# Performance work log

Measured on AMD Instinct MI355X. Metric: run time of the kernel, lower is better.

## Reference

```python
import jax, jax.numpy as jnp
import numpy as np

RADIUS, HMIN, HMAX, NSAMPLE = 0.05, -0.02, 0.04, 32
EPS = 1e-5


def setup_inputs() -> dict:
    key = jax.random.key(0)
    ks = jax.random.split(key, 6)
    B, N, C, OUT = 4, 2048, 256, 256
    seed_xyz_graspable = jax.random.uniform(ks[0], (B, N, 3), jnp.float32) * 0.2
    seed_features_graspable = jax.random.normal(ks[1], (B, C, N), jnp.float32)
    vp_rot = jax.random.normal(ks[2], (B, N, 3, 3), jnp.float32)
    W1 = jax.random.normal(ks[3], (OUT, 3 + C), jnp.float32) * 0.02
    W2 = jax.random.normal(ks[4], (OUT, OUT), jnp.float32) * 0.02
    return {
        "seed_xyz_graspable": seed_xyz_graspable,
        "seed_features_graspable": seed_features_graspable,
        "vp_rot": vp_rot,
        "W1": W1, "gamma1": jnp.ones((OUT,), jnp.float32), "beta1": jnp.zeros((OUT,), jnp.float32),
        "W2": W2, "gamma2": jnp.ones((OUT,), jnp.float32), "beta2": jnp.zeros((OUT,), jnp.float32),
    }


def _cylinder_query(xyz, rot):
    # xyz: (B,N,3), rot: (B,N,3,3); new_xyz == xyz.
    B, N, _ = xyz.shape
    d = xyz[:, None, :, :] - xyz[:, :, None, :]                  # (B,P,N,3) offsets to each candidate
    r = jnp.einsum('bpij,bpnj->bpni', rot, d)                    # rotate into cylinder frame (rot @ d)
    mask = (r[..., 1] ** 2 + r[..., 2] ** 2 < RADIUS ** 2) & (r[..., 0] > HMIN) & (r[..., 0] < HMAX)
    order = jnp.arange(N, dtype=jnp.int32)
    keys = jnp.where(mask, order, order + N)                     # in-cylinder points sort first, stable order
    _, idx = jax.lax.top_k(-keys, NSAMPLE)                       # first NSAMPLE indices satisfying the query
    valid = jnp.take_along_axis(mask, idx, axis=-1)
    first = idx[..., :1]
    any_valid = valid[..., :1]
    idx = jnp.where(valid, idx, jnp.where(any_valid, first, 0))  # pad with first hit like the CUDA kernel
    return idx                                                   # (B,P,NSAMPLE) int32


def _group(xyz, features, rot, idx):
    gxyz = jax.vmap(lambda a, i: a[i])(xyz, idx)                 # (B,P,S,3)
    gxyz = (gxyz - xyz[:, :, None, :]) / RADIUS                  # center on query + normalize_xyz
    gxyz = jnp.einsum('bpsj,bpjk->bpsk', gxyz, rot)              # rotate_xyz: grouped_xyz @ rot
    gfeat = jax.vmap(lambda f, i: f[:, i])(features, idx)        # (B,C,P,S)
    return jnp.concatenate([gxyz.transpose(0, 3, 1, 2), gfeat], axis=1)  # (B,3+C,P,S)


def _conv_bn_relu(x, W, gamma, beta):
    y = jnp.einsum('oc,bcps->bops', W, x)                        # 1x1 conv, no bias (bn=True)
    mu = y.mean(axis=(0, 2, 3), keepdims=True)
    var = y.var(axis=(0, 2, 3), keepdims=True)
    y = (y - mu) * jax.lax.rsqrt(var + EPS)
    y = y * gamma[None, :, None, None] + beta[None, :, None, None]
    return jax.nn.relu(y)


def reference(seed_xyz_graspable, seed_features_graspable, vp_rot, W1, gamma1, beta1, W2, gamma2, beta2):
    idx = _cylinder_query(seed_xyz_graspable, vp_rot)
    g = _group(seed_xyz_graspable, seed_features_graspable, vp_rot, idx)
    h = _conv_bn_relu(g, W1, gamma1, beta1)
    h = _conv_bn_relu(h, W2, gamma2, beta2)
    return h.max(axis=3)                                         # maxpool over nsample -> (B,OUT,P)
```

## Files before the change

### kernel.cpp

```cpp
#include <hip/hip_runtime.h>

typedef unsigned short u16;
typedef unsigned int u32;
typedef __attribute__((ext_vector_type(8))) short bf16x8;
typedef __attribute__((ext_vector_type(4))) float f32x4;

#define NPTS 2048
#define CFEAT 256
#define NS 32
#define MTOT 262144
#define GRID1 2048
#define GRID2 4096
#define INV_N (1.0f/262144.0f)

__device__ __forceinline__ float bf2f(u16 u) {
    union { u32 i; float f; } v; v.i = ((u32)u) << 16; return v.f;
}
__device__ __forceinline__ u16 f2bf(float f) {
    union { float f; u32 i; } v; v.f = f;
    u32 i = v.i;
    return (u16)((i + 0x7fffu + ((i >> 16) & 1u)) >> 16);
}

__device__ __forceinline__ void stage1k(u16* lds, const u16* g, int lane) {
    __builtin_amdgcn_global_load_lds((const __attribute__((address_space(1))) void*)(g + lane * 8),
                                     (__attribute__((address_space(3))) void*)lds, 16, 0, 0);
}

__global__ __launch_bounds__(256) void prep_k(const float* __restrict__ W1, const float* __restrict__ W2,
                                              u16* __restrict__ Wp1T, u16* __restrict__ Wp2T) {
    int o = blockIdx.x, t = threadIdx.x;
    int ks = t >> 5, kc = t & 31;
    Wp1T[(ks * 256 + o) * 32 + kc] = f2bf(W1[o * 259 + 3 + t]);
    Wp2T[(ks * 256 + o) * 32 + kc] = f2bf(W2[o * 256 + t]);
    if (t < 32) Wp1T[(8 * 256 + o) * 32 + t] = (t < 3) ? f2bf(W1[o * 259 + t]) : (u16)0;
}

__global__ __launch_bounds__(256) void query_k(const float* __restrict__ xyz, const float* __restrict__ rot,
                                               int* __restrict__ idx) {
    int pid = blockIdx.x * 4 + (threadIdx.x >> 6);
    int lane = threadIdx.x & 63;
    int b = pid >> 11, p = pid & 2047;
    const float* xb = xyz + (size_t)b * NPTS * 3;
    float px = xb[p * 3 + 0], py = xb[p * 3 + 1], pz = xb[p * 3 + 2];
    const float* rp = rot + (size_t)pid * 9;
    float r00 = rp[0], r01 = rp[1], r02 = rp[2];
    float r10 = rp[3], r11 = rp[4], r12 = rp[5];
    float r20 = rp[6], r21 = rp[7], r22 = rp[8];
    int cnt = 0, first = 0;
    for (int n0 = 0; n0 < NPTS && cnt < NS; n0 += 64) {
        int n = n0 + lane;
        float dx = __fsub_rn(xb[n * 3 + 0], px);
        float dy = __fsub_rn(xb[n * 3 + 1], py);
        float dz = __fsub_rn(xb[n * 3 + 2], pz);
        float a0 = __fadd_rn(__fadd_rn(__fmul_rn(r00, dx), __fmul_rn(r01, dy)), __fmul_rn(r02, dz));
        float a1 = __fadd_rn(__fadd_rn(__fmul_rn(r10, dx), __fmul_rn(r11, dy)), __fmul_rn(r12, dz));
        float a2 = __fadd_rn(__fadd_rn(__fmul_rn(r20, dx), __fmul_rn(r21, dy)), __fmul_rn(r22, dz));
        float t2 = __fadd_rn(__fmul_rn(a1, a1), __fmul_rn(a2, a2));
        bool valid = (t2 < 0.0025f) && (a0 > -0.02f) && (a0 < 0.04f);
        unsigned long long bal = __ballot(valid);
        if (cnt == 0 && bal) first = n0 + __builtin_ctzll(bal);
        int rank = __builtin_popcountll(bal & ((1ull << lane) - 1ull));
        int slot = cnt + rank;
        if (valid && slot < NS) idx[(size_t)pid * NS + slot] = n;
        cnt += __builtin_popcountll(bal);
    }
    int filled = cnt < NS ? cnt : NS;
    if (lane >= filled && lane < NS) idx[(size_t)pid * NS + lane] = (cnt > 0) ? first : 0;
}

__global__ __launch_bounds__(256) void featT_k(const float* __restrict__ feat, u16* __restrict__ featT) {
    __shared__ float sm[32 * 33];
    int b = blockIdx.z;
    int n0 = blockIdx.x * 32, c0 = blockIdx.y * 32;
    int t = threadIdx.x, x = t & 31, y = t >> 5;
    #pragma unroll
    for (int rr = 0; rr < 4; rr++) {
        int c = c0 + y + rr * 8;
        sm[(y + rr * 8) * 33 + x] = feat[((size_t)(b * CFEAT + c)) * NPTS + n0 + x];
    }
    __syncthreads();
    #pragma unroll
    for (int rr = 0; rr < 4; rr++) {
        int n = n0 + y + rr * 8;
        featT[((size_t)(b * NPTS + n)) * CFEAT + c0 + x] = f2bf(sm[x * 33 + (y + rr * 8)]);
    }
}

__global__ __launch_bounds__(256) void gxyz_k(const float* __restrict__ xyz, const float* __restrict__ rot,
                                              const int* __restrict__ idx, u16* __restrict__ gxyz) {
    int m = blockIdx.x * 256 + threadIdx.x;
    int pid = m >> 5;
    int b = pid >> 11, p = pid & 2047;
    int i = idx[m];
    const float* xb = xyz + (size_t)b * NPTS * 3;
    float dx = (xb[i * 3 + 0] - xb[p * 3 + 0]) * 20.0f;
    float dy = (xb[i * 3 + 1] - xb[p * 3 + 1]) * 20.0f;
    float dz = (xb[i * 3 + 2] - xb[p * 3 + 2]) * 20.0f;
    const float* rp = rot + (size_t)pid * 9;
    float g0 = dx * rp[0] + dy * rp[3] + dz * rp[6];
    float g1 = dx * rp[1] + dy * rp[4] + dz * rp[7];
    float g2 = dx * rp[2] + dy * rp[5] + dz * rp[8];
    uint2 v;
    v.x = (u32)f2bf(g0) | ((u32)f2bf(g1) << 16);
    v.y = (u32)f2bf(g2);
    *(uint2*)(gxyz + (size_t)m * 4) = v;
}

#define ASTR 40
__global__ __launch_bounds__(256, 2) void gemm1_k(
    const u16* __restrict__ featT, const u16* __restrict__ gxyz, const int* __restrict__ idx,
    const u16* __restrict__ Wp1T, float* __restrict__ psum, float* __restrict__ psq,
    uint2* __restrict__ y1f)
{
    __shared__ __attribute__((aligned(16))) u16 As[2][128 * ASTR];
    __shared__ __attribute__((aligned(16))) u16 Bs[2][8192];
    __shared__ int rowb[128];

    const int tid = threadIdx.x;
    const int lane = tid & 63, wave = tid >> 6;
    const int quad = lane >> 4, tl = lane & 15;
    const int wm = (wave & 1) * 64, wn = (wave >> 1) * 128;
    const int bx = blockIdx.x;
    const int m0 = bx * 128;
    const int srow = tid >> 1, shalf = tid & 1;

    if (tid < 128) {
        int m = m0 + tid;
        rowb[tid] = (m >> 16) * (NPTS * CFEAT) + idx[m] * CFEAT;
    }
    __syncthreads();

    {
        const u16* p = featT + rowb[srow] + shalf * 16;
        *(uint4*)(&As[0][srow * ASTR + shalf * 16]) = *(const uint4*)p;
        *(uint4*)(&As[0][srow * ASTR + shalf * 16 + 8]) = *(const uint4*)(p + 8);
    }
    #pragma unroll
    for (int c = 0; c < 4; c++)
        stage1k(&Bs[0][wave * 2048 + c * 512], Wp1T + wave * 2048 + c * 512, lane);

    f32x4 acc[4][8];
    #pragma unroll
    for (int i = 0; i < 4; i++)
        #pragma unroll
        for (int j = 0; j < 8; j++) acc[i][j] = (f32x4){0.f, 0.f, 0.f, 0.f};

    for (int ks = 0; ks < 9; ks++) {
        __syncthreads();
        const u16* Ab = As[ks & 1];
        const u16* Bb = Bs[ks & 1];
        bf16x8 af[4], bv[8];
        #pragma unroll
        for (int i = 0; i < 4; i++)
            af[i] = *(const bf16x8*)(Ab + (wm + i * 16 + tl) * ASTR + quad * 8);
        #pragma unroll
        for (int j = 0; j < 8; j++)
            bv[j] = *(const bf16x8*)(Bb + (wn + j * 16 + tl) * 32 + quad * 8);
        if (ks < 8) {
            u16* An = As[(ks + 1) & 1];
            u16* Bn = Bs[(ks + 1) & 1];
            const u16* gsrc = Wp1T + (ks + 1) * 8192;
            #pragma unroll
            for (int c = 0; c < 4; c++)
                stage1k(Bn + wave * 2048 + c * 512, gsrc + wave * 2048 + c * 512, lane);
            uint4 v0, v1;
            if (ks + 1 < 8) {
                const u16* p = featT + rowb[srow] + (ks + 1) * 32 + shalf * 16;
                v0 = *(const uint4*)p; v1 = *(const uint4*)(p + 8);
            } else {
                v0 = make_uint4(0, 0, 0, 0); v1 = v0;
                if (shalf == 0) {
                    uint2 g2 = *(const uint2*)(gxyz + (size_t)(m0 + srow) * 4);
                    v0.x = g2.x; v0.y = g2.y;
                }
            }
            *(uint4*)(An + srow * ASTR + shalf * 16) = v0;
            *(uint4*)(An + srow * ASTR + shalf * 16 + 8) = v1;
        }
        #pragma unroll
        for (int j = 0; j < 8; j++)
            #pragma unroll
            for (int i = 0; i < 4; i++)
                acc[i][j] = __builtin_amdgcn_mfma_f32_16x16x32_bf16(af[i], bv[j], acc[i][j], 0, 0, 0);
    }

    const int mb = bx * 2 + (wave & 1);
    #pragma unroll
    for (int j = 0; j < 8; j++) {
        const int cb = (wave >> 1) * 2 + (j >> 2);
        float s = 0.f, q2 = 0.f;
        #pragma unroll
        for (int i = 0; i < 4; i++) {
            float v0 = acc[i][j][0], v1 = acc[i][j][1], v2 = acc[i][j][2], v3 = acc[i][j][3];
            u32 lo = (u32)f2bf(v0) | ((u32)f2bf(v1) << 16);
            u32 hi = (u32)f2bf(v2) | ((u32)f2bf(v3) << 16);
            y1f[(((size_t)mb * 4 + cb) * 16 + i * 4 + (j & 3)) * 64 + lane] = make_uint2(lo, hi);
            v0 = bf2f((u16)(lo & 0xffff)); v1 = bf2f((u16)(lo >> 16));
            v2 = bf2f((u16)(hi & 0xffff)); v3 = bf2f((u16)(hi >> 16));
            s += v0 + v1 + v2 + v3;
            q2 += v0 * v0 + v1 * v1 + v2 * v2 + v3 * v3;
        }
        s += __shfl_xor(s, 16); s += __shfl_xor(s, 32);
        q2 += __shfl_xor(q2, 16); q2 += __shfl_xor(q2, 32);
        if (quad == 0) {
            int col = wn + j * 16 + tl;
            psum[(size_t)mb * 256 + col] = s;
            psq[(size_t)mb * 256 + col] = q2;
        }
    }
}

__global__ __launch_bounds__(256, 3) void gemm2_k(
    const uint2* __restrict__ y1f, const u16* __restrict__ Wp2T, const float* __restrict__ ab1,
    float* __restrict__ psum, float* __restrict__ psq,
    float* __restrict__ ymax, float* __restrict__ ymin)
{
    __shared__ __attribute__((aligned(16))) u16 Bs[8192];
    __shared__ __attribute__((aligned(16))) u16 y1s[64 * 264];
    const int tid = threadIdx.x;
    const int lane = tid & 63, wave = tid >> 6;
    const int quad = lane >> 4, tl = lane & 15;
    const int bx = blockIdx.x;

    #pragma unroll
    for (int j = 0; j < 4; j++) {
        int col = wave * 64 + j * 16 + tl;
        float a = ab1[col], bb = ab1[256 + col];
        #pragma unroll
        for (int i = 0; i < 4; i++) {
            uint2 v = y1f[((size_t)(bx * 4 + wave) * 16 + i * 4 + j) * 64 + lane];
            float f0 = bf2f((u16)(v.x & 0xffff)), f1 = bf2f((u16)(v.x >> 16));
            float f2 = bf2f((u16)(v.y & 0xffff)), f3 = bf2f((u16)(v.y >> 16));
            int rbi = (i * 16 + quad * 4) * 264 + col;
            y1s[rbi] = f2bf(fmaxf(fmaf(f0, a, bb), 0.f));
            y1s[rbi + 264] = f2bf(fmaxf(fmaf(f1, a, bb), 0.f));
            y1s[rbi + 528] = f2bf(fmaxf(fmaf(f2, a, bb), 0.f));
            y1s[rbi + 792] = f2bf(fmaxf(fmaf(f3, a, bb), 0.f));
        }
    }

    f32x4 acc2[4][4];
    #pragma unroll
    for (int i = 0; i < 4; i++)
        #pragma unroll
        for (int j = 0; j < 4; j++) acc2[i][j] = (f32x4){0.f, 0.f, 0.f, 0.f};

    for (int ks = 0; ks < 8; ks++) {
        const u16* gsrc = Wp2T + ks * 8192;
        #pragma unroll
        for (int c = 0; c < 4; c++)
            stage1k(Bs + wave * 2048 + c * 512, gsrc + wave * 2048 + c * 512, lane);
        __syncthreads();
        bf16x8 afv[4], bv[4];
        #pragma unroll
        for (int i = 0; i < 4; i++) afv[i] = *(const bf16x8*)(y1s + (i * 16 + tl) * 264 + ks * 32 + quad * 8);
        #pragma unroll
        for (int j = 0; j < 4; j++) bv[j] = *(const bf16x8*)(Bs + (wave * 64 + j * 16 + tl) * 32 + quad * 8);
        #pragma unroll
        for (int i = 0; i < 4; i++)
            #pragma unroll
            for (int j = 0; j < 4; j++)
                acc2[i][j] = __builtin_amdgcn_mfma_f32_16x16x32_bf16(afv[i], bv[j], acc2[i][j], 0, 0, 0);
        if (ks < 7) __syncthreads();
    }

    #pragma unroll
    for (int j = 0; j < 4; j++) {
        int col = wave * 64 + j * 16 + tl;
        float s = 0.f, q2 = 0.f;
        float mx0 = -3.0e38f, mn0 = 3.0e38f, mx1 = -3.0e38f, mn1 = 3.0e38f;
        #pragma unroll
        for (int i = 0; i < 4; i++)
            #pragma unroll
            for (int r = 0; r < 4; r++) {
                float v = acc2[i][j][r];
                s += v; q2 += v * v;
                if (i < 2) { mx0 = fmaxf(mx0, v); mn0 = fminf(mn0, v); }
                else       { mx1 = fmaxf(mx1, v); mn1 = fminf(mn1, v); }
            }
        s += __shfl_xor(s, 16); s += __shfl_xor(s, 32);
        q2 += __shfl_xor(q2, 16); q2 += __shfl_xor(q2, 32);
        mx0 = fmaxf(mx0, __shfl_xor(mx0, 16)); mx0 = fmaxf(mx0, __shfl_xor(mx0, 32));
        mn0 = fminf(mn0, __shfl_xor(mn0, 16)); mn0 = fminf(mn0, __shfl_xor(mn0, 32));
        mx1 = fmaxf(mx1, __shfl_xor(mx1, 16)); mx1 = fmaxf(mx1, __shfl_xor(mx1, 32));
        mn1 = fminf(mn1, __shfl_xor(mn1, 16)); mn1 = fminf(mn1, __shfl_xor(mn1, 32));
        if (quad == 0) {
            psum[(size_t)bx * 256 + col] = s;
            psq[(size_t)bx * 256 + col] = q2;
            size_t p0 = (size_t)(bx * 2) * 256 + col;
            size_t p1 = (size_t)(bx * 2 + 1) * 256 + col;
            ymax[p0] = mx0; ymin[p0] = mn0;
            ymax[p1] = mx1; ymin[p1] = mn1;
        }
    }
}

__global__ __launch_bounds__(256) void reduce_k(const float* __restrict__ psum, const float* __restrict__ psq,
                                                const float* __restrict__ gamma, const float* __restrict__ beta,
                                                float* __restrict__ ab) {
    __shared__ float red[8];
    int c = blockIdx.x, t = threadIdx.x;
    float s = 0.f, q = 0.f;
    for (int k = t; k < 4096; k += 256) { s += psum[(size_t)k * 256 + c]; q += psq[(size_t)k * 256 + c]; }
    #pragma unroll
    for (int o = 32; o >= 1; o >>= 1) { s += __shfl_xor(s, o); q += __shfl_xor(q, o); }
    int lane = t & 63, w = t >> 6;
    if (lane == 0) { red[w] = s; red[4 + w] = q; }
    __syncthreads();
    if (t == 0) {
        float S = red[0] + red[1] + red[2] + red[3];
        float Q = red[4] + red[5] + red[6] + red[7];
        float mu = S * INV_N;
        float var = Q * INV_N - mu * mu;
        float a = gamma[c] * rsqrtf(var + 1e-5f);
        ab[c] = a;
        ab[256 + c] = beta[c] - mu * a;
    }
}

__global__ __launch_bounds__(256) void final_k(const float* __restrict__ ymax, const float* __restrict__ ymin,
                                               const float* __restrict__ ab, float* __restrict__ out) {
    __shared__ float sm[32 * 33];
    int b = blockIdx.z;
    int n0 = blockIdx.x * 32, o0 = blockIdx.y * 32;
    int t = threadIdx.x, x = t & 31, y = t >> 5;
    #pragma unroll
    for (int rr = 0; rr < 4; rr++) {
        int n = n0 + y + rr * 8;
        int o = o0 + x;
        float a = ab[o], bb = ab[256 + o];
        size_t p = (size_t)(b * NPTS + n) * 256 + o;
        float v = (a >= 0.f) ? ymax[p] : ymin[p];
        sm[(y + rr * 8) * 33 + x] = fmaxf(fmaf(v, a, bb), 0.f);
    }
    __syncthreads();
    #pragma unroll
    for (int rr = 0; rr < 4; rr++)
        out[((size_t)(b * 256 + o0 + y + rr * 8)) * NPTS + n0 + x] = sm[x * 33 + (y + rr * 8)];
}

extern "C" void kernel_launch(void* const* d_in, const int* in_sizes, int n_in,
                              void* d_out, int out_size, void* d_ws, size_t ws_size,
                              hipStream_t stream) {
    const float* xyz    = (const float*)d_in[0];
    const float* feat   = (const float*)d_in[1];
    const float* rot    = (const float*)d_in[2];
    const float* W1     = (const float*)d_in[3];
    const float* gamma1 = (const float*)d_in[4];
    const float* beta1  = (const float*)d_in[5];
    const float* W2     = (const float*)d_in[6];
    const float* gamma2 = (const float*)d_in[7];
    const float* beta2  = (const float*)d_in[8];
    float* out = (float*)d_out;

    char* ws = (char*)d_ws;
    u16*   featT = (u16*)(ws + 0);
    int*   idx   = (int*)(ws + 4194304);
    u16*   gxyz  = (u16*)(ws + 5242880);
    u16*   Wp1T  = (u16*)(ws + 7340032);
    u16*   Wp2T  = (u16*)(ws + 7487488);
    float* ab1   = (float*)(ws + 7618560);
    float* ab2   = (float*)(ws + 7620608);
    float* psum  = (float*)(ws + 7622656);
    float* psq   = (float*)(ws + 11816960);
    float* ymax  = (float*)(ws + 16011264);
    float* ymin  = (float*)(ws + 24399872);
    uint2* y1f   = (uint2*)(ws + 32788480);

    prep_k<<<256, 256, 0, stream>>>(W1, W2, Wp1T, Wp2T);
    query_k<<<2048, 256, 0, stream>>>(xyz, rot, idx);
    featT_k<<<dim3(64, 8, 4), 256, 0, stream>>>(feat, featT);
    gxyz_k<<<1024, 256, 0, stream>>>(xyz, rot, idx, gxyz);

    gemm1_k<<<GRID1, 256, 0, stream>>>(featT, gxyz, idx, Wp1T, psum, psq, y1f);
    reduce_k<<<256, 256, 0, stream>>>(psum, psq, gamma1, beta1, ab1);
    gemm2_k<<<GRID2, 256, 0, stream>>>(y1f, Wp2T, ab1, psum, psq, ymax, ymin);
    reduce_k<<<256, 256, 0, stream>>>(psum, psq, gamma2, beta2, ab2);
    final_k<<<dim3(64, 8, 4), 256, 0, stream>>>(ymax, ymin, ab2, out);
}
```

Baseline: 257.4 us.

## Fuse gxyz into gemm1 and retile gemm2 with pipelined K-sliced y1 layout

The separate gxyz kernel is removed and its rotated neighbour offsets are computed inside gemm1 and kept in shared memory. gemm1 now writes y1 through shared memory into a K-sliced row-major layout. gemm2 is retiled to 128x256 blocks with double-buffered A and B staging, applying BN1 and ReLU while staging. This cuts a kernel launch and the gxyz round trip, and aims for better MFMA reuse in gemm2, at the cost of a larger gemm1 epilogue and more LDS and register pressure.

```diff
diff --git a/kernel.cpp b/kernel.cpp
--- a/kernel.cpp
+++ b/kernel.cpp
@@ -10,8 +10,9 @@
 #define NS 32
 #define MTOT 262144
 #define GRID1 2048
-#define GRID2 4096
 #define INV_N (1.0f/262144.0f)
+#define ASTR 40
+#define YSTR 260
 
 __device__ __forceinline__ float bf2f(u16 u) {
     union { u32 i; float f; } v; v.i = ((u32)u) << 16; return v.f;
@@ -87,35 +88,17 @@
     }
 }
 
-__global__ __launch_bounds__(256) void gxyz_k(const float* __restrict__ xyz, const float* __restrict__ rot,
-                                              const int* __restrict__ idx, u16* __restrict__ gxyz) {
-    int m = blockIdx.x * 256 + threadIdx.x;
-    int pid = m >> 5;
-    int b = pid >> 11, p = pid & 2047;
-    int i = idx[m];
-    const float* xb = xyz + (size_t)b * NPTS * 3;
-    float dx = (xb[i * 3 + 0] - xb[p * 3 + 0]) * 20.0f;
-    float dy = (xb[i * 3 + 1] - xb[p * 3 + 1]) * 20.0f;
-    float dz = (xb[i * 3 + 2] - xb[p * 3 + 2]) * 20.0f;
-    const float* rp = rot + (size_t)pid * 9;
-    float g0 = dx * rp[0] + dy * rp[3] + dz * rp[6];
-    float g1 = dx * rp[1] + dy * rp[4] + dz * rp[7];
-    float g2 = dx * rp[2] + dy * rp[5] + dz * rp[8];
-    uint2 v;
-    v.x = (u32)f2bf(g0) | ((u32)f2bf(g1) << 16);
-    v.y = (u32)f2bf(g2);
-    *(uint2*)(gxyz + (size_t)m * 4) = v;
-}
-
-#define ASTR 40
 __global__ __launch_bounds__(256, 2) void gemm1_k(
-    const u16* __restrict__ featT, const u16* __restrict__ gxyz, const int* __restrict__ idx,
+    const float* __restrict__ xyz, const float* __restrict__ rot,
+    const u16* __restrict__ featT, const int* __restrict__ idx,
     const u16* __restrict__ Wp1T, float* __restrict__ psum, float* __restrict__ psq,
-    uint2* __restrict__ y1f)
+    u16* __restrict__ y1t)
 {
-    __shared__ __attribute__((aligned(16))) u16 As[2][128 * ASTR];
-    __shared__ __attribute__((aligned(16))) u16 Bs[2][8192];
+    __shared__ __attribute__((aligned(16))) u16 smem[26624];
     __shared__ int rowb[128];
+    __shared__ uint2 gxs[128];
+    u16* As = smem;
+    u16* Bs = smem + 10240;
 
     const int tid = threadIdx.x;
     const int lane = tid & 63, wave = tid >> 6;
@@ -127,18 +110,28 @@
 
     if (tid < 128) {
         int m = m0 + tid;
-        rowb[tid] = (m >> 16) * (NPTS * CFEAT) + idx[m] * CFEAT;
+        int b = m >> 16, p = (m >> 5) & 2047, gi = idx[m];
+        rowb[tid] = b * (NPTS * CFEAT) + gi * CFEAT;
+        const float* xb = xyz + (size_t)b * NPTS * 3;
+        float dx = (xb[gi * 3 + 0] - xb[p * 3 + 0]) * 20.0f;
+        float dy = (xb[gi * 3 + 1] - xb[p * 3 + 1]) * 20.0f;
+        float dz = (xb[gi * 3 + 2] - xb[p * 3 + 2]) * 20.0f;
+        const float* rp = rot + (size_t)(m >> 5) * 9;
+        float g0 = dx * rp[0] + dy * rp[3] + dz * rp[6];
+        float g1 = dx * rp[1] + dy * rp[4] + dz * rp[7];
+        float g2 = dx * rp[2] + dy * rp[5] + dz * rp[8];
+        gxs[tid] = make_uint2((u32)f2bf(g0) | ((u32)f2bf(g1) << 16), (u32)f2bf(g2));
     }
     __syncthreads();
 
     {
         const u16* p = featT + rowb[srow] + shalf * 16;
-        *(uint4*)(&As[0][srow * ASTR + shalf * 16]) = *(const uint4*)p;
-        *(uint4*)(&As[0][srow * ASTR + shalf * 16 + 8]) = *(const uint4*)(p + 8);
+        *(uint4*)(As + srow * ASTR + shalf * 16) = *(const uint4*)p;
+        *(uint4*)(As + srow * ASTR + shalf * 16 + 8) = *(const uint4*)(p + 8);
     }
     #pragma unroll
     for (int c = 0; c < 4; c++)
-        stage1k(&Bs[0][wave * 2048 + c * 512], Wp1T + wave * 2048 + c * 512, lane);
+        stage1k(Bs + wave * 2048 + c * 512, Wp1T + wave * 2048 + c * 512, lane);
 
     f32x4 acc[4][8];
     #pragma unroll
@@ -148,8 +141,8 @@
 
     for (int ks = 0; ks < 9; ks++) {
         __syncthreads();
-        const u16* Ab = As[ks & 1];
-        const u16* Bb = Bs[ks & 1];
+        const u16* Ab = As + (ks & 1) * 5120;
+        const u16* Bb = Bs + (ks & 1) * 8192;
         bf16x8 af[4], bv[8];
         #pragma unroll
         for (int i = 0; i < 4; i++)
@@ -158,8 +151,8 @@
         for (int j = 0; j < 8; j++)
             bv[j] = *(const bf16x8*)(Bb + (wn + j * 16 + tl) * 32 + quad * 8);
         if (ks < 8) {
-            u16* An = As[(ks + 1) & 1];
-            u16* Bn = Bs[(ks + 1) & 1];
+            u16* An = As + ((ks + 1) & 1) * 5120;
+            u16* Bn = Bs + ((ks + 1) & 1) * 8192;
             const u16* gsrc = Wp1T + (ks + 1) * 8192;
             #pragma unroll
             for (int c = 0; c < 4; c++)
@@ -171,7 +164,7 @@
             } else {
                 v0 = make_uint4(0, 0, 0, 0); v1 = v0;
                 if (shalf == 0) {
-                    uint2 g2 = *(const uint2*)(gxyz + (size_t)(m0 + srow) * 4);
+                    uint2 g2 = gxs[srow];
                     v0.x = g2.x; v0.y = g2.y;
                 }
             }
@@ -185,96 +178,134 @@
                 acc[i][j] = __builtin_amdgcn_mfma_f32_16x16x32_bf16(af[i], bv[j], acc[i][j], 0, 0, 0);
     }
 
-    const int mb = bx * 2 + (wave & 1);
-    #pragma unroll
-    for (int j = 0; j < 8; j++) {
-        const int cb = (wave >> 1) * 2 + (j >> 2);
-        float s = 0.f, q2 = 0.f;
-        #pragma unroll
-        for (int i = 0; i < 4; i++) {
-            float v0 = acc[i][j][0], v1 = acc[i][j][1], v2 = acc[i][j][2], v3 = acc[i][j][3];
-            u32 lo = (u32)f2bf(v0) | ((u32)f2bf(v1) << 16);
-            u32 hi = (u32)f2bf(v2) | ((u32)f2bf(v3) << 16);
-            y1f[(((size_t)mb * 4 + cb) * 16 + i * 4 + (j & 3)) * 64 + lane] = make_uint2(lo, hi);
-            v0 = bf2f((u16)(lo & 0xffff)); v1 = bf2f((u16)(lo >> 16));
-            v2 = bf2f((u16)(hi & 0xffff)); v3 = bf2f((u16)(hi >> 16));
-            s += v0 + v1 + v2 + v3;
-            q2 += v0 * v0 + v1 * v1 + v2 * v2 + v3 * v3;
-        }
-        s += __shfl_xor(s, 16); s += __shfl_xor(s, 32);
-        q2 += __shfl_xor(q2, 16); q2 += __shfl_xor(q2, 32);
-        if (quad == 0) {
-            int col = wn + j * 16 + tl;
-            psum[(size_t)mb * 256 + col] = s;
-            psq[(size_t)mb * 256 + col] = q2;
-        }
-    }
-}
-
-__global__ __launch_bounds__(256, 3) void gemm2_k(
-    const uint2* __restrict__ y1f, const u16* __restrict__ Wp2T, const float* __restrict__ ab1,
+    u16* y1s = smem;
+    const int lrow = tid >> 2, c4 = tid & 3;
+    #pragma unroll
+    for (int r = 0; r < 2; r++) {
+        __syncthreads();
+        if ((wave & 1) == r) {
+            const int mb = bx * 2 + r;
+            #pragma unroll
+            for (int j = 0; j < 8; j++) {
+                int col = wn + j * 16 + tl;
+                float s = 0.f, q2 = 0.f;
+                #pragma unroll
+                for (int i = 0; i < 4; i++)
+                    #pragma unroll
+                    for (int rr = 0; rr < 4; rr++) {
+                        u16 h = f2bf(acc[i][j][rr]);
+                        y1s[(i * 16 + quad * 4 + rr) * YSTR + col] = h;
+                        float v = bf2f(h); s += v; q2 += v * v;
+                    }
+                s += __shfl_xor(s, 16); s += __shfl_xor(s, 32);
+                q2 += __shfl_xor(q2, 16); q2 += __shfl_xor(q2, 32);
+                if (quad == 0) {
+                    psum[(size_t)mb * 256 + col] = s;
+                    psq[(size_t)mb * 256 + col] = q2;
+                }
+            }
+        }
+        __syncthreads();
+        #pragma unroll
+        for (int ks = 0; ks < 8; ks++) {
+            const u16* sp = y1s + lrow * YSTR + ks * 32 + c4 * 8;
+            uint2 a0 = *(const uint2*)sp;
+            uint2 a1 = *(const uint2*)(sp + 4);
+            *(uint4*)(y1t + (((size_t)bx * 8 + ks) * 128 + r * 64 + lrow) * 32 + c4 * 8) =
+                make_uint4(a0.x, a0.y, a1.x, a1.y);
+        }
+    }
+}
+
+__global__ __launch_bounds__(256, 2) void gemm2_k(
+    const u16* __restrict__ y1t, const u16* __restrict__ Wp2T, const float* __restrict__ ab1,
     float* __restrict__ psum, float* __restrict__ psq,
     float* __restrict__ ymax, float* __restrict__ ymin)
 {
-    __shared__ __attribute__((aligned(16))) u16 Bs[8192];
-    __shared__ __attribute__((aligned(16))) u16 y1s[64 * 264];
+    __shared__ __attribute__((aligned(16))) u16 smem[26624];
+    __shared__ float coef[512];
+    u16* As = smem;
+    u16* Bs = smem + 10240;
+
     const int tid = threadIdx.x;
     const int lane = tid & 63, wave = tid >> 6;
     const int quad = lane >> 4, tl = lane & 15;
+    const int wm = (wave & 1) * 64, wn = (wave >> 1) * 128;
     const int bx = blockIdx.x;
-
-    #pragma unroll
-    for (int j = 0; j < 4; j++) {
-        int col = wave * 64 + j * 16 + tl;
-        float a = ab1[col], bb = ab1[256 + col];
-        #pragma unroll
-        for (int i = 0; i < 4; i++) {
-            uint2 v = y1f[((size_t)(bx * 4 + wave) * 16 + i * 4 + j) * 64 + lane];
-            float f0 = bf2f((u16)(v.x & 0xffff)), f1 = bf2f((u16)(v.x >> 16));
-            float f2 = bf2f((u16)(v.y & 0xffff)), f3 = bf2f((u16)(v.y >> 16));
-            int rbi = (i * 16 + quad * 4) * 264 + col;
-            y1s[rbi] = f2bf(fmaxf(fmaf(f0, a, bb), 0.f));
-            y1s[rbi + 264] = f2bf(fmaxf(fmaf(f1, a, bb), 0.f));
-            y1s[rbi + 528] = f2bf(fmaxf(fmaf(f2, a, bb), 0.f));
-            y1s[rbi + 792] = f2bf(fmaxf(fmaf(f3, a, bb), 0.f));
-        }
-    }
-
-    f32x4 acc2[4][4];
+    const int srow = tid >> 1, shalf = tid & 1;
+    const u16* Abase = y1t + (size_t)bx * 32768;
+
+    ((float2*)coef)[tid] = ((const float2*)ab1)[tid];
+    __syncthreads();
+
+    auto stageA = [&](int ks, u16* An) {
+        const u16* pp = Abase + (ks * 128 + srow) * 32 + shalf * 16;
+        uint4 v0 = *(const uint4*)pp, v1 = *(const uint4*)(pp + 8);
+        const float4* ca = (const float4*)(coef + ks * 32 + shalf * 16);
+        const float4* cb = (const float4*)(coef + 256 + ks * 32 + shalf * 16);
+        u32 w[8] = {v0.x, v0.y, v0.z, v0.w, v1.x, v1.y, v1.z, v1.w};
+        u32 o[8];
+        #pragma unroll
+        for (int g = 0; g < 4; g++) {
+            float4 a4 = ca[g], b4 = cb[g];
+            float f0 = fmaxf(fmaf(bf2f((u16)(w[2*g]   & 0xffff)), a4.x, b4.x), 0.f);
+            float f1 = fmaxf(fmaf(bf2f((u16)(w[2*g]   >> 16)),    a4.y, b4.y), 0.f);
+            float f2 = fmaxf(fmaf(bf2f((u16)(w[2*g+1] & 0xffff)), a4.z, b4.z), 0.f);
+            float f3 = fmaxf(fmaf(bf2f((u16)(w[2*g+1] >> 16)),    a4.w, b4.w), 0.f);
+            o[2*g]   = (u32)f2bf(f0) | ((u32)f2bf(f1) << 16);
+            o[2*g+1] = (u32)f2bf(f2) | ((u32)f2bf(f3) << 16);
+        }
+        *(uint4*)(An + srow * ASTR + shalf * 16)     = make_uint4(o[0], o[1], o[2], o[3]);
+        *(uint4*)(An + srow * ASTR + shalf * 16 + 8) = make_uint4(o[4], o[5], o[6], o[7]);
+    };
+
+    stageA(0, As);
+    #pragma unroll
+    for (int c = 0; c < 4; c++)
+        stage1k(Bs + wave * 2048 + c * 512, Wp2T + wave * 2048 + c * 512, lane);
+
+    f32x4 acc[4][8];
     #pragma unroll
     for (int i = 0; i < 4; i++)
         #pragma unroll
-        for (int j = 0; j < 4; j++) acc2[i][j] = (f32x4){0.f, 0.f, 0.f, 0.f};
+        for (int j = 0; j < 8; j++) acc[i][j] = (f32x4){0.f, 0.f, 0.f, 0.f};
 
     for (int ks = 0; ks < 8; ks++) {
-        const u16* gsrc = Wp2T + ks * 8192;
-        #pragma unroll
-        for (int c = 0; c < 4; c++)
-            stage1k(Bs + wave * 2048 + c * 512, gsrc + wave * 2048 + c * 512, lane);
         __syncthreads();
-        bf16x8 afv[4], bv[4];
-        #pragma unroll
-        for (int i = 0; i < 4; i++) afv[i] = *(const bf16x8*)(y1s + (i * 16 + tl) * 264 + ks * 32 + quad * 8);
-        #pragma unroll
-        for (int j = 0; j < 4; j++) bv[j] = *(const bf16x8*)(Bs + (wave * 64 + j * 16 + tl) * 32 + quad * 8);
+        const u16* Ab = As + (ks & 1) * 5120;
+        const u16* Bb = Bs + (ks & 1) * 8192;
+        bf16x8 af[4], bv[8];
         #pragma unroll
         for (int i = 0; i < 4; i++)
-            #pragma unroll
-            for (int j = 0; j < 4; j++)
-                acc2[i][j] = __builtin_amdgcn_mfma_f32_16x16x32_bf16(afv[i], bv[j], acc2[i][j], 0, 0, 0);
-        if (ks < 7) __syncthreads();
-    }
-
-    #pragma unroll
-    for (int j = 0; j < 4; j++) {
-        int col = wave * 64 + j * 16 + tl;
+            af[i] = *(const bf16x8*)(Ab + (wm + i * 16 + tl) * ASTR + quad * 8);
+        #pragma unroll
+        for (int j = 0; j < 8; j++)
+            bv[j] = *(const bf16x8*)(Bb + (wn + j * 16 + tl) * 32 + quad * 8);
+        if (ks < 7) {
+            stageA(ks + 1, As + ((ks + 1) & 1) * 5120);
+            const u16* gsrc = Wp2T + (ks + 1) * 8192;
+            u16* Bn = Bs + ((ks + 1) & 1) * 8192;
+            #pragma unroll
+            for (int c = 0; c < 4; c++)
+                stage1k(Bn + wave * 2048 + c * 512, gsrc + wave * 2048 + c * 512, lane);
+        }
+        #pragma unroll
+        for (int j = 0; j < 8; j++)
+            #pragma unroll
+            for (int i = 0; i < 4; i++)
+                acc[i][j] = __builtin_amdgcn_mfma_f32_16x16x32_bf16(af[i], bv[j], acc[i][j], 0, 0, 0);
+    }
+
+    #pragma unroll
+    for (int j = 0; j < 8; j++) {
+        int col = wn + j * 16 + tl;
         float s = 0.f, q2 = 0.f;
         float mx0 = -3.0e38f, mn0 = 3.0e38f, mx1 = -3.0e38f, mn1 = 3.0e38f;
         #pragma unroll
         for (int i = 0; i < 4; i++)
             #pragma unroll
-            for (int r = 0; r < 4; r++) {
-                float v = acc2[i][j][r];
+            for (int rr = 0; rr < 4; rr++) {
+                float v = acc[i][j][rr];
                 s += v; q2 += v * v;
                 if (i < 2) { mx0 = fmaxf(mx0, v); mn0 = fminf(mn0, v); }
                 else       { mx1 = fmaxf(mx1, v); mn1 = fminf(mn1, v); }
@@ -286,12 +317,12 @@
         mx1 = fmaxf(mx1, __shfl_xor(mx1, 16)); mx1 = fmaxf(mx1, __shfl_xor(mx1, 32));
         mn1 = fminf(mn1, __shfl_xor(mn1, 16)); mn1 = fminf(mn1, __shfl_xor(mn1, 32));
         if (quad == 0) {
-            psum[(size_t)bx * 256 + col] = s;
-            psq[(size_t)bx * 256 + col] = q2;
-            size_t p0 = (size_t)(bx * 2) * 256 + col;
-            size_t p1 = (size_t)(bx * 2 + 1) * 256 + col;
+            int mb = bx * 2 + (wave & 1);
+            psum[(size_t)mb * 256 + col] = s;
+            psq[(size_t)mb * 256 + col] = q2;
+            size_t p0 = ((size_t)bx * 4 + (wave & 1) * 2) * 256 + col;
             ymax[p0] = mx0; ymin[p0] = mn0;
-            ymax[p1] = mx1; ymin[p1] = mn1;
+            ymax[p0 + 256] = mx1; ymin[p0 + 256] = mn1;
         }
     }
 }
@@ -357,7 +388,6 @@
     char* ws = (char*)d_ws;
     u16*   featT = (u16*)(ws + 0);
     int*   idx   = (int*)(ws + 4194304);
-    u16*   gxyz  = (u16*)(ws + 5242880);
     u16*   Wp1T  = (u16*)(ws + 7340032);
     u16*   Wp2T  = (u16*)(ws + 7487488);
     float* ab1   = (float*)(ws + 7618560);
@@ -366,16 +396,15 @@
     float* psq   = (float*)(ws + 11816960);
     float* ymax  = (float*)(ws + 16011264);
     float* ymin  = (float*)(ws + 24399872);
-    uint2* y1f   = (uint2*)(ws + 32788480);
+    u16*   y1t   = (u16*)(ws + 32788480);
 
     prep_k<<<256, 256, 0, stream>>>(W1, W2, Wp1T, Wp2T);
     query_k<<<2048, 256, 0, stream>>>(xyz, rot, idx);
     featT_k<<<dim3(64, 8, 4), 256, 0, stream>>>(feat, featT);
-    gxyz_k<<<1024, 256, 0, stream>>>(xyz, rot, idx, gxyz);
-
-    gemm1_k<<<GRID1, 256, 0, stream>>>(featT, gxyz, idx, Wp1T, psum, psq, y1f);
+
+    gemm1_k<<<GRID1, 256, 0, stream>>>(xyz, rot, featT, idx, Wp1T, psum, psq, y1t);
     reduce_k<<<256, 256, 0, stream>>>(psum, psq, gamma1, beta1, ab1);
-    gemm2_k<<<GRID2, 256, 0, stream>>>(y1f, Wp2T, ab1, psum, psq, ymax, ymin);
+    gemm2_k<<<GRID1, 256, 0, stream>>>(y1t, Wp2T, ab1, psum, psq, ymax, ymin);
     reduce_k<<<256, 256, 0, stream>>>(psum, psq, gamma2, beta2, ab2);
     final_k<<<dim3(64, 8, 4), 256, 0, stream>>>(ymax, ymin, ab2, out);
 }
```

After: 261.8 us. No clear change (+1.7%).
